# Performance work log

Measured on AMD Instinct MI355X. Metric: run time of the kernel, lower is better.

The kernel has to match this reference:

```python
import jax, jax.numpy as jnp
import numpy as np

N_HEAD = 16
NEG_MASK = -10000.0

def setup_inputs() -> dict:
    key = jax.random.key(0)
    ks = jax.random.split(key, 5)
    B, S, E = 2, 1024, 1024
    return {
        "hidden_states": jax.random.normal(ks[0], (B, S, E), dtype=jnp.float32),
        "W_attn": jax.random.normal(ks[1], (E, 3 * E), dtype=jnp.float32) * (1.0 / np.sqrt(E)),
        "b_attn": jax.random.normal(ks[2], (3 * E,), dtype=jnp.float32) * 0.02,
        "W_proj": jax.random.normal(ks[3], (E, E), dtype=jnp.float32) * (1.0 / np.sqrt(E)),
        "b_proj": jax.random.normal(ks[4], (E,), dtype=jnp.float32) * 0.02,
    }

def reference(hidden_states, W_attn, b_attn, W_proj, b_proj):
    B, S, E = hidden_states.shape
    H = N_HEAD
    D = E // H
    qkv = hidden_states @ W_attn + b_attn            # [B,S,3E]
    q, k, v = jnp.split(qkv, 3, axis=2)              # each [B,S,E]
    def split_heads(x):
        return x.reshape(B, S, H, D).transpose(0, 2, 1, 3)  # [B,H,S,D]
    q, k, v = split_heads(q), split_heads(k), split_heads(v)
    scale = 1.0 / float(D) ** 0.5
    scores = jnp.einsum('bhqd,bhkd->bhqk', q, k) * scale    # [B,H,S,S]
    causal = jnp.tril(jnp.ones((S, S), dtype=bool))
    scores = jnp.where(causal, scores, jnp.asarray(NEG_MASK, scores.dtype))
    attn_weights = jax.nn.softmax(scores, axis=-1)          # [B,H,S,S]
    attn_out = jnp.einsum('bhqk,bhkd->bhqd', attn_weights, v)
    attn_out = attn_out.transpose(0, 2, 1, 3).reshape(B, S, E)
    attn_out = attn_out @ W_proj + b_proj
    return attn_out, attn_weights
```

## Files before the change

### kernel.cpp

```cpp
#include <hip/hip_runtime.h>

#define SDIM 1024
#define EDIM 1024
#define BDIM 2
#define HDIM 16
#define DDIM 64
#define MDIM 2048
#define N3   3072

typedef __attribute__((ext_vector_type(8))) short bf16x8;
typedef __attribute__((ext_vector_type(4))) float f32x4;

__device__ __forceinline__ ushort f2bf(float f) {
  union { float f; unsigned u; } x; x.f = f;
  unsigned u = x.u;
  u += 0x7FFFu + ((u >> 16) & 1u);
  return (ushort)(u >> 16);
}

__global__ __launch_bounds__(256) void cast_bf16_kernel(
    const float* __restrict__ in, ushort* __restrict__ out, int n) {
  int i = (blockIdx.x * 256 + threadIdx.x) * 4;
  if (i < n) {
    float4 v = *reinterpret_cast<const float4*>(&in[i]);
    ushort4 o;
    o.x = f2bf(v.x); o.y = f2bf(v.y); o.z = f2bf(v.z); o.w = f2bf(v.w);
    *reinterpret_cast<ushort4*>(&out[i]) = o;
  }
}

__global__ __launch_bounds__(256) void transpose_cast_kernel(
    const float* __restrict__ W, ushort* __restrict__ WT, int ncols) {
  __shared__ float t[32][33];
  int n0 = blockIdx.x * 32, k0 = blockIdx.y * 32;
  int tx = threadIdx.x & 31, ty = threadIdx.x >> 5;
#pragma unroll
  for (int j = 0; j < 4; ++j)
    t[ty + j * 8][tx] = W[(size_t)(k0 + ty + j * 8) * ncols + n0 + tx];
  __syncthreads();
#pragma unroll
  for (int j = 0; j < 4; ++j)
    WT[(size_t)(n0 + ty + j * 8) * EDIM + k0 + tx] = f2bf(t[tx][ty + j * 8]);
}

__global__ __launch_bounds__(256) void qkv_gemm_mfma(
    const ushort* __restrict__ Abf, const ushort* __restrict__ WT,
    const float* __restrict__ bias, float* __restrict__ Qo,
    float* __restrict__ KTo, ushort* __restrict__ VTo) {
  const int K = EDIM;
  __shared__ ushort As[128][40];
  __shared__ ushort Bs[128][40];
  int bm = blockIdx.y * 128, bn = blockIdx.x * 128;
  int tid = threadIdx.x;
  int lane = tid & 63, wave = tid >> 6;
  int wr = (wave >> 1) * 64, wc = (wave & 1) * 64;
  int fr = lane & 15;
  int ko = (lane >> 4) * 8;

  f32x4 acc[4][4] = {};

  for (int k0 = 0; k0 < K; k0 += 32) {
#pragma unroll
    for (int i = 0; i < 2; ++i) {
      int c = tid + i * 256;
      int r = c >> 2, o = (c & 3) * 8;
      *reinterpret_cast<float4*>(&As[r][o]) =
          *reinterpret_cast<const float4*>(&Abf[(size_t)(bm + r) * K + k0 + o]);
      *reinterpret_cast<float4*>(&Bs[r][o]) =
          *reinterpret_cast<const float4*>(&WT[(size_t)(bn + r) * K + k0 + o]);
    }
    __syncthreads();
    bf16x8 a[4], b[4];
#pragma unroll
    for (int f = 0; f < 4; ++f) {
      a[f] = *reinterpret_cast<const bf16x8*>(&As[wr + f * 16 + fr][ko]);
      b[f] = *reinterpret_cast<const bf16x8*>(&Bs[wc + f * 16 + fr][ko]);
    }
#pragma unroll
    for (int i = 0; i < 4; ++i)
#pragma unroll
      for (int j = 0; j < 4; ++j)
        acc[i][j] = __builtin_amdgcn_mfma_f32_16x16x32_bf16(a[i], b[j],
                                                            acc[i][j], 0, 0, 0);
    __syncthreads();
  }

  int rbase = (lane >> 4) << 2;
#pragma unroll
  for (int i = 0; i < 4; ++i)
#pragma unroll
    for (int j = 0; j < 4; ++j)
#pragma unroll
      for (int r = 0; r < 4; ++r) {
        int m = bm + wr + i * 16 + rbase + r;
        int n = bn + wc + j * 16 + (lane & 15);
        float val = acc[i][j][r] + bias[n];
        int b = m >> 10, s = m & 1023;
        int which = n >> 10;
        int e = n & 1023;
        int h = e >> 6, d = e & 63;
        int bh = b * HDIM + h;
        if (which == 0) {
          Qo[(((size_t)bh << 10) + s) * DDIM + d] = val;
        } else if (which == 1) {
          KTo[((size_t)(bh * DDIM + d) << 10) + s] = val;
        } else {
          VTo[((size_t)(bh * DDIM + d) << 10) + s] = f2bf(val);
        }
      }
}

__global__ __launch_bounds__(256) void attn_softmax_kernel(
    const float* __restrict__ Q, const float* __restrict__ KT,
    float* __restrict__ Wout) {
  __shared__ float qs[8][64];
  __shared__ float redA[8][4];
  __shared__ float redB[8][4];
  int bh = blockIdx.y;
  int q0 = blockIdx.x * 8;
  int tid = threadIdx.x;
  int lane = tid & 63, wid = tid >> 6;
  const float* Qb = Q + (((size_t)bh) << 10) * DDIM;
  const float* Kb = KT + ((size_t)bh << 16);
  if (tid < 128) {
    int r = tid >> 4, c = (tid & 15) << 2;
    *reinterpret_cast<float4*>(&qs[r][c]) =
        *reinterpret_cast<const float4*>(&Qb[(size_t)(q0 + r) * DDIM + c]);
  }
  __syncthreads();

  float sc[4][8];
#pragma unroll
  for (int j = 0; j < 4; ++j)
#pragma unroll
    for (int qi = 0; qi < 8; ++qi) sc[j][qi] = 0.f;

  const float* kpb = Kb + (tid << 2);

  float4 kc0 = *reinterpret_cast<const float4*>(kpb + (0 << 10));
  float4 kc1 = *reinterpret_cast<const float4*>(kpb + (1 << 10));
  float4 kc2 = *reinterpret_cast<const float4*>(kpb + (2 << 10));
  float4 kc3 = *reinterpret_cast<const float4*>(kpb + (3 << 10));

#pragma unroll 1
  for (int d4 = 0; d4 < 16; ++d4) {
    int nd = (((d4 + 1) & 15) << 2);
    float4 kn0 = *reinterpret_cast<const float4*>(kpb + ((size_t)(nd + 0) << 10));
    float4 kn1 = *reinterpret_cast<const float4*>(kpb + ((size_t)(nd + 1) << 10));
    float4 kn2 = *reinterpret_cast<const float4*>(kpb + ((size_t)(nd + 2) << 10));
    float4 kn3 = *reinterpret_cast<const float4*>(kpb + ((size_t)(nd + 3) << 10));
#pragma unroll
    for (int qi = 0; qi < 8; ++qi) {
      float4 q4 = *reinterpret_cast<const float4*>(&qs[qi][d4 << 2]);
      sc[0][qi] += q4.x * kc0.x + q4.y * kc1.x + q4.z * kc2.x + q4.w * kc3.x;
      sc[1][qi] += q4.x * kc0.y + q4.y * kc1.y + q4.z * kc2.y + q4.w * kc3.y;
      sc[2][qi] += q4.x * kc0.z + q4.y * kc1.z + q4.z * kc2.z + q4.w * kc3.z;
      sc[3][qi] += q4.x * kc0.w + q4.y * kc1.w + q4.z * kc2.w + q4.w * kc3.w;
    }
    kc0 = kn0; kc1 = kn1; kc2 = kn2; kc3 = kn3;
  }

  const float scale = 0.125f;
  int kbase = tid << 2;
  float rmax[8];
#pragma unroll
  for (int qi = 0; qi < 8; ++qi) {
    int qg = q0 + qi;
    float m = -3.4e38f;
#pragma unroll
    for (int j = 0; j < 4; ++j) {
      float s = sc[j][qi] * scale;
      sc[j][qi] = s;
      if (kbase + j <= qg) m = fmaxf(m, s);
    }
#pragma unroll
    for (int off = 32; off; off >>= 1) m = fmaxf(m, __shfl_xor(m, off));
    if (lane == 0) redA[qi][wid] = m;
  }
  __syncthreads();
#pragma unroll
  for (int qi = 0; qi < 8; ++qi)
    rmax[qi] = fmaxf(fmaxf(redA[qi][0], redA[qi][1]),
                     fmaxf(redA[qi][2], redA[qi][3]));
#pragma unroll
  for (int qi = 0; qi < 8; ++qi) {
    int qg = q0 + qi;
    float s = 0.f;
#pragma unroll
    for (int j = 0; j < 4; ++j) {
      float e = (kbase + j <= qg) ? __expf(sc[j][qi] - rmax[qi]) : 0.f;
      sc[j][qi] = e;
      s += e;
    }
#pragma unroll
    for (int off = 32; off; off >>= 1) s += __shfl_xor(s, off);
    if (lane == 0) redB[qi][wid] = s;
  }
  __syncthreads();
#pragma unroll
  for (int qi = 0; qi < 8; ++qi) {
    float inv = 1.0f / (redB[qi][0] + redB[qi][1] + redB[qi][2] + redB[qi][3]);
    float* Wr = Wout + ((((size_t)bh << 10) + q0 + qi) << 10);
    float4 w4 = {sc[0][qi] * inv, sc[1][qi] * inv, sc[2][qi] * inv, sc[3][qi] * inv};
    *reinterpret_cast<float4*>(&Wr[kbase]) = w4;
  }
}

__global__ __launch_bounds__(256) void pv_mfma(
    const float* __restrict__ P, const ushort* __restrict__ VT,
    ushort* __restrict__ ctx_bf) {
  __shared__ ushort As[128][40];
  __shared__ ushort Bs[64][40];
  int bh = blockIdx.y, bm = blockIdx.x * 128;
  int b = bh >> 4, h = bh & 15;
  const float* Pb = P + ((size_t)bh << 20);
  const ushort* Vb = VT + ((size_t)bh << 16);
  int tid = threadIdx.x;
  int lane = tid & 63, wave = tid >> 6;
  int wr = (wave >> 1) * 64, wc = (wave & 1) * 32;
  int fr = lane & 15;
  int ko = (lane >> 4) * 8;

  f32x4 acc[4][2] = {};

  for (int k0 = 0; k0 < SDIM; k0 += 32) {
#pragma unroll
    for (int i = 0; i < 4; ++i) {
      int c = tid + i * 256;
      int r = c >> 3, o = (c & 7) * 4;
      float4 v = *reinterpret_cast<const float4*>(&Pb[((size_t)(bm + r) << 10) + k0 + o]);
      ushort4 u;
      u.x = f2bf(v.x); u.y = f2bf(v.y); u.z = f2bf(v.z); u.w = f2bf(v.w);
      *reinterpret_cast<ushort4*>(&As[r][o]) = u;
    }
    {
      int r = tid >> 2, o = (tid & 3) * 8;
      *reinterpret_cast<float4*>(&Bs[r][o]) =
          *reinterpret_cast<const float4*>(&Vb[((size_t)r << 10) + k0 + o]);
    }
    __syncthreads();
    bf16x8 a[4], bb[2];
#pragma unroll
    for (int f = 0; f < 4; ++f)
      a[f] = *reinterpret_cast<const bf16x8*>(&As[wr + f * 16 + fr][ko]);
#pragma unroll
    for (int f = 0; f < 2; ++f)
      bb[f] = *reinterpret_cast<const bf16x8*>(&Bs[wc + f * 16 + fr][ko]);
#pragma unroll
    for (int i = 0; i < 4; ++i)
#pragma unroll
      for (int j = 0; j < 2; ++j)
        acc[i][j] = __builtin_amdgcn_mfma_f32_16x16x32_bf16(a[i], bb[j],
                                                            acc[i][j], 0, 0, 0);
    __syncthreads();
  }

  int rbase = (lane >> 4) << 2;
#pragma unroll
  for (int i = 0; i < 4; ++i)
#pragma unroll
    for (int j = 0; j < 2; ++j)
#pragma unroll
      for (int r = 0; r < 4; ++r) {
        int m = bm + wr + i * 16 + rbase + r;
        int n = wc + j * 16 + (lane & 15);
        ctx_bf[(size_t)(b * SDIM + m) * EDIM + h * DDIM + n] = f2bf(acc[i][j][r]);
      }
}

__global__ __launch_bounds__(256) void proj_gemm_mfma(
    const ushort* __restrict__ Abf, const ushort* __restrict__ WT,
    const float* __restrict__ bias, float* __restrict__ Out) {
  const int K = EDIM;
  __shared__ ushort As[128][40];
  __shared__ ushort Bs[128][40];
  int bm = blockIdx.y * 128, bn = blockIdx.x * 128;
  int tid = threadIdx.x;
  int lane = tid & 63, wave = tid >> 6;
  int wr = (wave >> 1) * 64, wc = (wave & 1) * 64;
  int fr = lane & 15;
  int ko = (lane >> 4) * 8;

  f32x4 acc[4][4] = {};

  for (int k0 = 0; k0 < K; k0 += 32) {
#pragma unroll
    for (int i = 0; i < 2; ++i) {
      int c = tid + i * 256;
      int r = c >> 2, o = (c & 3) * 8;
      *reinterpret_cast<float4*>(&As[r][o]) =
          *reinterpret_cast<const float4*>(&Abf[(size_t)(bm + r) * K + k0 + o]);
      *reinterpret_cast<float4*>(&Bs[r][o]) =
          *reinterpret_cast<const float4*>(&WT[(size_t)(bn + r) * K + k0 + o]);
    }
    __syncthreads();
    bf16x8 a[4], b[4];
#pragma unroll
    for (int f = 0; f < 4; ++f) {
      a[f] = *reinterpret_cast<const bf16x8*>(&As[wr + f * 16 + fr][ko]);
      b[f] = *reinterpret_cast<const bf16x8*>(&Bs[wc + f * 16 + fr][ko]);
    }
#pragma unroll
    for (int i = 0; i < 4; ++i)
#pragma unroll
      for (int j = 0; j < 4; ++j)
        acc[i][j] = __builtin_amdgcn_mfma_f32_16x16x32_bf16(a[i], b[j],
                                                            acc[i][j], 0, 0, 0);
    __syncthreads();
  }

  int rbase = (lane >> 4) << 2;
#pragma unroll
  for (int i = 0; i < 4; ++i)
#pragma unroll
    for (int j = 0; j < 4; ++j)
#pragma unroll
      for (int r = 0; r < 4; ++r) {
        int m = bm + wr + i * 16 + rbase + r;
        int n = bn + wc + j * 16 + (lane & 15);
        Out[(size_t)m * EDIM + n] = acc[i][j][r] + bias[n];
      }
}

extern "C" void kernel_launch(void* const* d_in, const int* in_sizes, int n_in,
                              void* d_out, int out_size, void* d_ws, size_t ws_size,
                              hipStream_t stream) {
  const float* hs     = (const float*)d_in[0];
  const float* W_attn = (const float*)d_in[1];
  const float* b_attn = (const float*)d_in[2];
  const float* W_proj = (const float*)d_in[3];
  const float* b_proj = (const float*)d_in[4];

  float* out_attn = (float*)d_out;
  float* out_w    = (float*)d_out + (size_t)MDIM * EDIM;

  const size_t QSZ = (size_t)BDIM * HDIM * SDIM * DDIM;
  float* Q   = (float*)d_ws;
  float* KT  = Q + QSZ;
  ushort* VT = (ushort*)(KT + QSZ);
  ushort* ctx_bf = VT + QSZ;
  ushort* Abf = ctx_bf + (size_t)MDIM * EDIM;
  ushort* WTa = Abf + (size_t)MDIM * EDIM;
  ushort* WpT = WTa + (size_t)N3 * EDIM;

  cast_bf16_kernel<<<2048, 256, 0, stream>>>(hs, Abf, MDIM * EDIM);
  transpose_cast_kernel<<<dim3(N3 / 32, EDIM / 32), 256, 0, stream>>>(
      W_attn, WTa, N3);
  transpose_cast_kernel<<<dim3(EDIM / 32, EDIM / 32), 256, 0, stream>>>(
      W_proj, WpT, EDIM);
  qkv_gemm_mfma<<<dim3(N3 / 128, MDIM / 128), 256, 0, stream>>>(
      Abf, WTa, b_attn, Q, KT, VT);
  attn_softmax_kernel<<<dim3(SDIM / 8, BDIM * HDIM), 256, 0, stream>>>(
      Q, KT, out_w);
  pv_mfma<<<dim3(SDIM / 128, BDIM * HDIM), 256, 0, stream>>>(
      out_w, VT, ctx_bf);
  proj_gemm_mfma<<<dim3(EDIM / 128, MDIM / 128), 256, 0, stream>>>(
      ctx_bf, WpT, b_proj, out_attn);
}
```

Measured before the change: 338.6 us.

## Compute attention scores with bf16 MFMA, two-pass online softmax, causal tile skipping

The QKV GEMM now stores Q and K as bf16 in row-major head layout instead of fp32 with K transposed. The scalar-FMA scores/softmax kernel is replaced by an MFMA kernel. It first computes running max and sum over the causal key tiles, then recomputes the scores to write normalized weights, and writes zeros for the fully masked tiles without computing them. This removes the fp32 scalar dot-product cost and the work on masked tiles, at the price of computing QK twice and using bf16 precision for the scores. The weight stores are also less coalesced, scattered per lane in MFMA fragment order.

```diff
diff --git a/kernel.cpp b/kernel.cpp
--- a/kernel.cpp
+++ b/kernel.cpp
@@ -45,8 +45,8 @@
 
 __global__ __launch_bounds__(256) void qkv_gemm_mfma(
     const ushort* __restrict__ Abf, const ushort* __restrict__ WT,
-    const float* __restrict__ bias, float* __restrict__ Qo,
-    float* __restrict__ KTo, ushort* __restrict__ VTo) {
+    const float* __restrict__ bias, ushort* __restrict__ Qo,
+    ushort* __restrict__ Ko, ushort* __restrict__ VTo) {
   const int K = EDIM;
   __shared__ ushort As[128][40];
   __shared__ ushort Bs[128][40];
@@ -101,108 +101,137 @@
         int h = e >> 6, d = e & 63;
         int bh = b * HDIM + h;
         if (which == 0) {
-          Qo[(((size_t)bh << 10) + s) * DDIM + d] = val;
+          Qo[(((size_t)bh << 10) + s) * DDIM + d] = f2bf(val);
         } else if (which == 1) {
-          KTo[((size_t)(bh * DDIM + d) << 10) + s] = val;
+          Ko[(((size_t)bh << 10) + s) * DDIM + d] = f2bf(val);
         } else {
           VTo[((size_t)(bh * DDIM + d) << 10) + s] = f2bf(val);
         }
       }
 }
 
-__global__ __launch_bounds__(256) void attn_softmax_kernel(
-    const float* __restrict__ Q, const float* __restrict__ KT,
+__global__ __launch_bounds__(256) void attn_fused_kernel(
+    const ushort* __restrict__ Qbf, const ushort* __restrict__ Kbf,
     float* __restrict__ Wout) {
-  __shared__ float qs[8][64];
-  __shared__ float redA[8][4];
-  __shared__ float redB[8][4];
+  __shared__ ushort Ks[128][72];
   int bh = blockIdx.y;
-  int q0 = blockIdx.x * 8;
+  int q0 = blockIdx.x * 64;
   int tid = threadIdx.x;
-  int lane = tid & 63, wid = tid >> 6;
-  const float* Qb = Q + (((size_t)bh) << 10) * DDIM;
-  const float* Kb = KT + ((size_t)bh << 16);
-  if (tid < 128) {
-    int r = tid >> 4, c = (tid & 15) << 2;
-    *reinterpret_cast<float4*>(&qs[r][c]) =
-        *reinterpret_cast<const float4*>(&Qb[(size_t)(q0 + r) * DDIM + c]);
-  }
-  __syncthreads();
-
-  float sc[4][8];
-#pragma unroll
-  for (int j = 0; j < 4; ++j)
-#pragma unroll
-    for (int qi = 0; qi < 8; ++qi) sc[j][qi] = 0.f;
-
-  const float* kpb = Kb + (tid << 2);
-
-  float4 kc0 = *reinterpret_cast<const float4*>(kpb + (0 << 10));
-  float4 kc1 = *reinterpret_cast<const float4*>(kpb + (1 << 10));
-  float4 kc2 = *reinterpret_cast<const float4*>(kpb + (2 << 10));
-  float4 kc3 = *reinterpret_cast<const float4*>(kpb + (3 << 10));
-
-#pragma unroll 1
-  for (int d4 = 0; d4 < 16; ++d4) {
-    int nd = (((d4 + 1) & 15) << 2);
-    float4 kn0 = *reinterpret_cast<const float4*>(kpb + ((size_t)(nd + 0) << 10));
-    float4 kn1 = *reinterpret_cast<const float4*>(kpb + ((size_t)(nd + 1) << 10));
-    float4 kn2 = *reinterpret_cast<const float4*>(kpb + ((size_t)(nd + 2) << 10));
-    float4 kn3 = *reinterpret_cast<const float4*>(kpb + ((size_t)(nd + 3) << 10));
-#pragma unroll
-    for (int qi = 0; qi < 8; ++qi) {
-      float4 q4 = *reinterpret_cast<const float4*>(&qs[qi][d4 << 2]);
-      sc[0][qi] += q4.x * kc0.x + q4.y * kc1.x + q4.z * kc2.x + q4.w * kc3.x;
-      sc[1][qi] += q4.x * kc0.y + q4.y * kc1.y + q4.z * kc2.y + q4.w * kc3.y;
-      sc[2][qi] += q4.x * kc0.z + q4.y * kc1.z + q4.z * kc2.z + q4.w * kc3.z;
-      sc[3][qi] += q4.x * kc0.w + q4.y * kc1.w + q4.z * kc2.w + q4.w * kc3.w;
-    }
-    kc0 = kn0; kc1 = kn1; kc2 = kn2; kc3 = kn3;
+  int lane = tid & 63, wave = tid >> 6;
+  int qw = q0 + wave * 16;
+  const ushort* Qb = Qbf + (((size_t)bh) << 10) * DDIM;
+  const ushort* Kb = Kbf + (((size_t)bh) << 10) * DDIM;
+
+  bf16x8 aq[2];
+  {
+    int qrow = qw + (lane & 15);
+#pragma unroll
+    for (int ds = 0; ds < 2; ++ds)
+      aq[ds] = *reinterpret_cast<const bf16x8*>(
+          &Qb[(size_t)qrow * DDIM + ds * 32 + ((lane >> 4) << 3)]);
   }
 
   const float scale = 0.125f;
-  int kbase = tid << 2;
-  float rmax[8];
-#pragma unroll
-  for (int qi = 0; qi < 8; ++qi) {
-    int qg = q0 + qi;
-    float m = -3.4e38f;
-#pragma unroll
-    for (int j = 0; j < 4; ++j) {
-      float s = sc[j][qi] * scale;
-      sc[j][qi] = s;
-      if (kbase + j <= qg) m = fmaxf(m, s);
-    }
-#pragma unroll
-    for (int off = 32; off; off >>= 1) m = fmaxf(m, __shfl_xor(m, off));
-    if (lane == 0) redA[qi][wid] = m;
-  }
-  __syncthreads();
-#pragma unroll
-  for (int qi = 0; qi < 8; ++qi)
-    rmax[qi] = fmaxf(fmaxf(redA[qi][0], redA[qi][1]),
-                     fmaxf(redA[qi][2], redA[qi][3]));
-#pragma unroll
-  for (int qi = 0; qi < 8; ++qi) {
-    int qg = q0 + qi;
-    float s = 0.f;
-#pragma unroll
-    for (int j = 0; j < 4; ++j) {
-      float e = (kbase + j <= qg) ? __expf(sc[j][qi] - rmax[qi]) : 0.f;
-      sc[j][qi] = e;
-      s += e;
-    }
-#pragma unroll
-    for (int off = 32; off; off >>= 1) s += __shfl_xor(s, off);
-    if (lane == 0) redB[qi][wid] = s;
-  }
-  __syncthreads();
-#pragma unroll
-  for (int qi = 0; qi < 8; ++qi) {
-    float inv = 1.0f / (redB[qi][0] + redB[qi][1] + redB[qi][2] + redB[qi][3]);
-    float* Wr = Wout + ((((size_t)bh << 10) + q0 + qi) << 10);
-    float4 w4 = {sc[0][qi] * inv, sc[1][qi] * inv, sc[2][qi] * inv, sc[3][qi] * inv};
-    *reinterpret_cast<float4*>(&Wr[kbase]) = w4;
+  int rq = (lane >> 4) << 2;
+  float m[4], l[4];
+#pragma unroll
+  for (int r = 0; r < 4; ++r) { m[r] = -3.4e38f; l[r] = 0.f; }
+
+  int ntA = (q0 >> 7) + 1;
+
+  for (int kt = 0; kt < ntA; ++kt) {
+    __syncthreads();
+#pragma unroll
+    for (int i = 0; i < 4; ++i) {
+      int c = tid + i * 256;
+      int r = c >> 3, o = (c & 7) * 8;
+      *reinterpret_cast<float4*>(&Ks[r][o]) =
+          *reinterpret_cast<const float4*>(&Kb[(size_t)(kt * 128 + r) * DDIM + o]);
+    }
+    __syncthreads();
+    f32x4 acc[8];
+#pragma unroll
+    for (int nf = 0; nf < 8; ++nf) {
+      bf16x8 b0 = *reinterpret_cast<const bf16x8*>(
+          &Ks[nf * 16 + (lane & 15)][(lane >> 4) << 3]);
+      bf16x8 b1 = *reinterpret_cast<const bf16x8*>(
+          &Ks[nf * 16 + (lane & 15)][32 + ((lane >> 4) << 3)]);
+      f32x4 z = {0.f, 0.f, 0.f, 0.f};
+      z = __builtin_amdgcn_mfma_f32_16x16x32_bf16(aq[0], b0, z, 0, 0, 0);
+      z = __builtin_amdgcn_mfma_f32_16x16x32_bf16(aq[1], b1, z, 0, 0, 0);
+      acc[nf] = z;
+    }
+    int kc = kt * 128 + (lane & 15);
+#pragma unroll
+    for (int r = 0; r < 4; ++r) {
+      int q = qw + rq + r;
+      float sv[8], tmax = -3.4e38f;
+#pragma unroll
+      for (int nf = 0; nf < 8; ++nf) {
+        float s = acc[nf][r] * scale;
+        sv[nf] = (kc + nf * 16 <= q) ? s : -3.4e38f;
+        tmax = fmaxf(tmax, sv[nf]);
+      }
+#pragma unroll
+      for (int off = 8; off; off >>= 1) tmax = fmaxf(tmax, __shfl_xor(tmax, off));
+      float mn = fmaxf(m[r], tmax);
+      float ps = 0.f;
+#pragma unroll
+      for (int nf = 0; nf < 8; ++nf) ps += __expf(sv[nf] - mn);
+#pragma unroll
+      for (int off = 8; off; off >>= 1) ps += __shfl_xor(ps, off);
+      l[r] = l[r] * __expf(m[r] - mn) + ps;
+      m[r] = mn;
+    }
+  }
+
+  float linv[4];
+#pragma unroll
+  for (int r = 0; r < 4; ++r) linv[r] = 1.0f / l[r];
+
+  float* Wr = Wout + ((size_t)bh << 20);
+
+  for (int kt = 0; kt < ntA; ++kt) {
+    __syncthreads();
+#pragma unroll
+    for (int i = 0; i < 4; ++i) {
+      int c = tid + i * 256;
+      int r = c >> 3, o = (c & 7) * 8;
+      *reinterpret_cast<float4*>(&Ks[r][o]) =
+          *reinterpret_cast<const float4*>(&Kb[(size_t)(kt * 128 + r) * DDIM + o]);
+    }
+    __syncthreads();
+    f32x4 acc[8];
+#pragma unroll
+    for (int nf = 0; nf < 8; ++nf) {
+      bf16x8 b0 = *reinterpret_cast<const bf16x8*>(
+          &Ks[nf * 16 + (lane & 15)][(lane >> 4) << 3]);
+      bf16x8 b1 = *reinterpret_cast<const bf16x8*>(
+          &Ks[nf * 16 + (lane & 15)][32 + ((lane >> 4) << 3)]);
+      f32x4 z = {0.f, 0.f, 0.f, 0.f};
+      z = __builtin_amdgcn_mfma_f32_16x16x32_bf16(aq[0], b0, z, 0, 0, 0);
+      z = __builtin_amdgcn_mfma_f32_16x16x32_bf16(aq[1], b1, z, 0, 0, 0);
+      acc[nf] = z;
+    }
+    int kc = kt * 128 + (lane & 15);
+#pragma unroll
+    for (int nf = 0; nf < 8; ++nf) {
+      int k = kc + nf * 16;
+#pragma unroll
+      for (int r = 0; r < 4; ++r) {
+        int q = qw + rq + r;
+        float w = (k <= q) ? __expf(acc[nf][r] * scale - m[r]) * linv[r] : 0.f;
+        Wr[((size_t)q << 10) + k] = w;
+      }
+    }
+  }
+  for (int kt = ntA; kt < 8; ++kt) {
+    int kc = kt * 128 + (lane & 15);
+#pragma unroll
+    for (int nf = 0; nf < 8; ++nf)
+#pragma unroll
+      for (int r = 0; r < 4; ++r)
+        Wr[((size_t)(qw + rq + r) << 10) + kc + nf * 16] = 0.f;
   }
 }
 
@@ -335,9 +364,9 @@
   float* out_w    = (float*)d_out + (size_t)MDIM * EDIM;
 
   const size_t QSZ = (size_t)BDIM * HDIM * SDIM * DDIM;
-  float* Q   = (float*)d_ws;
-  float* KT  = Q + QSZ;
-  ushort* VT = (ushort*)(KT + QSZ);
+  ushort* Qbf = (ushort*)d_ws;
+  ushort* Kbf = Qbf + QSZ;
+  ushort* VT  = Kbf + QSZ;
   ushort* ctx_bf = VT + QSZ;
   ushort* Abf = ctx_bf + (size_t)MDIM * EDIM;
   ushort* WTa = Abf + (size_t)MDIM * EDIM;
@@ -349,9 +378,9 @@
   transpose_cast_kernel<<<dim3(EDIM / 32, EDIM / 32), 256, 0, stream>>>(
       W_proj, WpT, EDIM);
   qkv_gemm_mfma<<<dim3(N3 / 128, MDIM / 128), 256, 0, stream>>>(
-      Abf, WTa, b_attn, Q, KT, VT);
-  attn_softmax_kernel<<<dim3(SDIM / 8, BDIM * HDIM), 256, 0, stream>>>(
-      Q, KT, out_w);
+      Abf, WTa, b_attn, Qbf, Kbf, VT);
+  attn_fused_kernel<<<dim3(SDIM / 64, BDIM * HDIM), 256, 0, stream>>>(
+      Qbf, Kbf, out_w);
   pv_mfma<<<dim3(SDIM / 128, BDIM * HDIM), 256, 0, stream>>>(
       out_w, VT, ctx_bf);
   proj_gemm_mfma<<<dim3(EDIM / 128, MDIM / 128), 256, 0, stream>>>(
```

Result: faster. 275.4 us (-18.7%).
